# Performance work log

Hardware: AMD Instinct MI355X
Metric: run time of the kernel (lower is better)

Reference implementation:

```python
import jax, jax.numpy as jnp
import numpy as np

B, C, HC, H, W = 4, 512, 64, 64, 64


def _spectral_norm(Wm, u):
    # one torch-style power iteration; u,v are treated as constants (detached)
    v = Wm.T @ u
    v = v / jnp.maximum(jnp.linalg.norm(v), 1e-12)
    u2 = Wm @ v
    u2 = u2 / jnp.maximum(jnp.linalg.norm(u2), 1e-12)
    u2 = jax.lax.stop_gradient(u2)
    v = jax.lax.stop_gradient(v)
    sigma = u2 @ (Wm @ v)
    return Wm / sigma


def setup_inputs() -> dict:
    key = jax.random.key(0)
    ks = jax.random.split(key, 14)
    return {
        "x": jax.random.normal(ks[0], (B, C, H, W), jnp.float32),
        "Wf": jax.random.normal(ks[1], (HC, C), jnp.float32) * 0.05,
        "bf": jax.random.normal(ks[2], (HC,), jnp.float32) * 0.05,
        "Wg": jax.random.normal(ks[3], (HC, C), jnp.float32) * 0.05,
        "bg": jax.random.normal(ks[4], (HC,), jnp.float32) * 0.05,
        "Wh": jax.random.normal(ks[5], (HC, C), jnp.float32) * 0.05,
        "bh": jax.random.normal(ks[6], (HC,), jnp.float32) * 0.05,
        "Wv": jax.random.normal(ks[7], (C, HC), jnp.float32) * 0.05,
        "bv": jax.random.normal(ks[8], (C,), jnp.float32) * 0.05,
        "uf": jax.random.normal(ks[9], (HC,), jnp.float32),
        "ug": jax.random.normal(ks[10], (HC,), jnp.float32),
        "uh": jax.random.normal(ks[11], (HC,), jnp.float32),
        "uv": jax.random.normal(ks[12], (C,), jnp.float32),
        "gamma": jax.random.normal(ks[13], (1,), jnp.float32),
    }


def reference(x, Wf, bf, Wg, bg, Wh, bh, Wv, bv, uf, ug, uh, uv, gamma):
    nb, nc, imgh, imgw = x.shape
    n = imgh * imgw
    xf = x.reshape(nb, nc, n)  # [B, C, N]
    Wf_sn = _spectral_norm(Wf, uf)
    Wg_sn = _spectral_norm(Wg, ug)
    Wh_sn = _spectral_norm(Wh, uh)
    Wv_sn = _spectral_norm(Wv, uv)
    # 1x1 convs are per-pixel GEMMs
    f = jnp.einsum('kc,bcn->bkn', Wf_sn, xf) + bf[:, None]  # [B, HC, N]
    g = jnp.einsum('kc,bcn->bkn', Wg_sn, xf) + bg[:, None]
    h = jnp.einsum('kc,bcn->bkn', Wh_sn, xf) + bh[:, None]
    s = jnp.einsum('bkn,bkm->bnm', f, g)       # [B, N, N] scores
    beta = jax.nn.softmax(s, axis=-1)
    o = jnp.einsum('bnm,bkm->bkn', beta, h)    # [B, HC, N] (already transposed)
    out = jnp.einsum('ck,bkn->bcn', Wv_sn, o) + bv[:, None]
    out = out.reshape(nb, nc, imgh, imgw)
    return gamma[0] * out + x
```

## Files before the change

kernel.cpp:

```cpp
#include <hip/hip_runtime.h>
#include <hip/hip_bf16.h>

typedef __attribute__((ext_vector_type(8))) short short8;
typedef __attribute__((ext_vector_type(4))) float floatx4;
typedef __attribute__((ext_vector_type(16))) float floatx16;
typedef unsigned short ushortt;

#define LOG2E 1.4426950408889634f

__device__ __forceinline__ float fast_exp2(float x) {
    return __builtin_amdgcn_exp2f(x);
}
__device__ __forceinline__ ushortt f2bf(float f) {
    unsigned int u = __float_as_uint(f);
    u += 0x7fffu + ((u >> 16) & 1u);
    return (ushortt)(u >> 16);
}
__device__ __forceinline__ unsigned int f2bf_pk(float a, float b) {
    float2 t; t.x = a; t.y = b;
    __hip_bfloat162 h = __float22bfloat162_rn(t);
    return *reinterpret_cast<unsigned int*>(&h);
}
__device__ __forceinline__ float bf2f(ushortt h) {
    return __uint_as_float(((unsigned int)h) << 16);
}

__device__ __forceinline__ float block_sum(float v, float* red) {
    #pragma unroll
    for (int off = 32; off > 0; off >>= 1) v += __shfl_down(v, off);
    int wid = threadIdx.x >> 6, ln = threadIdx.x & 63;
    __syncthreads();
    if (ln == 0) red[wid] = v;
    __syncthreads();
    return red[0] + red[1] + red[2] + red[3];
}

__global__ __launch_bounds__(256) void sigma_kernel(
    const float* __restrict__ Wf, const float* __restrict__ uf,
    const float* __restrict__ Wg, const float* __restrict__ ug,
    const float* __restrict__ Wh, const float* __restrict__ uh,
    const float* __restrict__ Wv, const float* __restrict__ uv,
    float* __restrict__ sig) {
    __shared__ float tv[512];
    __shared__ float tvp[256];
    __shared__ float zpart[256];
    __shared__ float red[4];
    const int mat = blockIdx.x, tid = threadIdx.x;

    if (mat < 3) {
        const float* W = (mat == 0) ? Wf : ((mat == 1) ? Wg : Wh);
        const float* u = (mat == 0) ? uf : ((mat == 1) ? ug : uh);
        for (int c = tid; c < 512; c += 256) {
            float s0 = 0.f;
            #pragma unroll 8
            for (int r = 0; r < 64; ++r) s0 += W[r * 512 + c] * u[r];
            tv[c] = s0;
        }
        __syncthreads();
        float p = tv[tid] * tv[tid] + tv[tid + 256] * tv[tid + 256];
        float nt2 = block_sum(p, red);
        float nt = fmaxf(sqrtf(nt2), 1e-12f);
        {
            int r = tid & 63, qq = tid >> 6;
            const float* Wr = W + r * 512 + qq * 128;
            const float* tq = tv + qq * 128;
            float part = 0.f;
            #pragma unroll 16
            for (int c = 0; c < 128; ++c) part += Wr[c] * tq[c];
            zpart[tid] = part;
        }
        __syncthreads();
        if (tid < 64) {
            float z = zpart[tid] + zpart[tid + 64] + zpart[tid + 128] + zpart[tid + 192];
            z = z * z;
            #pragma unroll
            for (int off = 32; off > 0; off >>= 1) z += __shfl_xor(z, off);
            if (tid == 0) sig[mat] = sqrtf(z) / nt;
        }
    } else {
        const float* W = Wv; const float* u = uv;
        {
            int c = tid & 63, rs = tid >> 6;
            float s0 = 0.f;
            #pragma unroll 8
            for (int r = rs * 128; r < rs * 128 + 128; ++r) s0 += W[r * 64 + c] * u[r];
            tvp[tid] = s0;
        }
        __syncthreads();
        if (tid < 64) tv[tid] = tvp[tid] + tvp[tid + 64] + tvp[tid + 128] + tvp[tid + 192];
        __syncthreads();
        float t = (tid < 64) ? tv[tid] : 0.f;
        float nt2 = block_sum(t * t, red);
        float nt = fmaxf(sqrtf(nt2), 1e-12f);
        {
            const float* w1 = W + (size_t)tid * 64;
            const float* w2 = W + (size_t)(tid + 256) * 64;
            float z1 = 0.f, z2 = 0.f;
            #pragma unroll 8
            for (int c = 0; c < 64; ++c) {
                float tc = tv[c];
                z1 += w1[c] * tc;
                z2 += w2[c] * tc;
            }
            float zp = z1 * z1 + z2 * z2;
            float z2t = block_sum(zp, red);
            if (tid == 0) sig[3] = sqrtf(z2t) / nt;
        }
    }
}

__global__ __launch_bounds__(256) void prep_w_kernel(
    const float* __restrict__ Wf, const float* __restrict__ Wg,
    const float* __restrict__ Wh, const float* __restrict__ Wv,
    const float* __restrict__ sig,
    ushortt* __restrict__ wqkv, ushortt* __restrict__ wvb) {
    int idx = blockIdx.x * 256 + threadIdx.x;
    if (idx < 98304) {
        int k = idx >> 9, c = idx & 511;
        int which = k >> 6;
        const float* W = (which == 0) ? Wf : ((which == 1) ? Wg : Wh);
        float inv = 1.0f / sig[which];
        wqkv[idx] = f2bf(W[(k & 63) * 512 + c] * inv);
    } else {
        int o = idx - 98304;
        wvb[o] = f2bf(Wv[o] / sig[3]);
    }
}

__global__ __launch_bounds__(256, 4) void qkv_kernel(
    const float* __restrict__ x, const ushortt* __restrict__ wqkv,
    const float* __restrict__ bfv, const float* __restrict__ bgv,
    const float* __restrict__ bhv,
    ushortt* __restrict__ Qb, ushortt* __restrict__ Kb, ushortt* __restrict__ Vt) {
    __shared__ unsigned int xs[2048];
    const int tid = threadIdx.x;
    const int n0 = blockIdx.x * 32, b = blockIdx.y;
    const int lane = tid & 63, w = tid >> 6;
    const int strip = w & 1, ksel = w >> 1;
    const int q = lane >> 4, l15 = lane & 15;
    const int sn = tid & 31, sg = tid >> 5;

    floatx4 acc[6];
    #pragma unroll
    for (int kt = 0; kt < 6; ++kt) acc[kt] = (floatx4){0.f, 0.f, 0.f, 0.f};

    const float* xb = x + ((size_t)b * 512) * 4096 + n0 + sn;
    const int sslot = sn * 32 + ((sg ^ (sn & 7)) << 2);
    float2 pre[4];
    #pragma unroll
    for (int i = 0; i < 4; ++i) {
        int c = sg * 8 + 2 * i;
        pre[i].x = xb[(size_t)c * 4096];
        pre[i].y = xb[(size_t)(c + 1) * 4096];
    }
    {
        uint4 pk;
        pk.x = f2bf_pk(pre[0].x, pre[0].y);
        pk.y = f2bf_pk(pre[1].x, pre[1].y);
        pk.z = f2bf_pk(pre[2].x, pre[2].y);
        pk.w = f2bf_pk(pre[3].x, pre[3].y);
        *reinterpret_cast<uint4*>(&xs[sslot]) = pk;
    }
    #pragma unroll
    for (int i = 0; i < 4; ++i) {
        int c = 64 + sg * 8 + 2 * i;
        pre[i].x = xb[(size_t)c * 4096];
        pre[i].y = xb[(size_t)(c + 1) * 4096];
    }

    for (int it = 0; it < 8; ++it) {
        __syncthreads();
        if (it < 7) {
            uint4 pk;
            pk.x = f2bf_pk(pre[0].x, pre[0].y);
            pk.y = f2bf_pk(pre[1].x, pre[1].y);
            pk.z = f2bf_pk(pre[2].x, pre[2].y);
            pk.w = f2bf_pk(pre[3].x, pre[3].y);
            *reinterpret_cast<uint4*>(&xs[(((it + 1) & 1) << 10) + sslot]) = pk;
        }
        if (it < 6) {
            #pragma unroll
            for (int i = 0; i < 4; ++i) {
                int c = (it + 2) * 64 + sg * 8 + 2 * i;
                pre[i].x = xb[(size_t)c * 4096];
                pre[i].y = xb[(size_t)(c + 1) * 4096];
            }
        }
        const int c0 = it * 64;
        const unsigned int* xr = &xs[((it & 1) << 10) + (16 * strip + l15) * 32];
        #pragma unroll
        for (int kc = 0; kc < 2; ++kc) {
            union { uint4 v; short8 s8; } af;
            af.v = *reinterpret_cast<const uint4*>(&xr[((4 * kc + q) ^ (l15 & 7)) << 2]);
            #pragma unroll
            for (int kt = 0; kt < 6; ++kt) {
                short8 bb = *reinterpret_cast<const short8*>(
                    &wqkv[(size_t)(ksel * 96 + kt * 16 + l15) * 512 + c0 + kc * 32 + q * 8]);
                acc[kt] = __builtin_amdgcn_mfma_f32_16x16x32_bf16(af.s8, bb, acc[kt], 0, 0, 0);
            }
        }
    }

    const int nloc = n0 + 16 * strip + 4 * q;
    if (ksel == 0) {
        #pragma unroll
        for (int kt = 0; kt < 4; ++kt) {
            int k = kt * 16 + l15;
            float bb = bfv[k];
            #pragma unroll
            for (int r = 0; r < 4; ++r)
                Qb[((size_t)b * 4096 + nloc + r) * 64 + k] = f2bf((acc[kt][r] + bb) * LOG2E);
        }
        #pragma unroll
        for (int kt = 4; kt < 6; ++kt) {
            int k = (kt - 4) * 16 + l15;
            float bb = bgv[k];
            #pragma unroll
            for (int r = 0; r < 4; ++r)
                Kb[((size_t)b * 4096 + nloc + r) * 64 + k] = f2bf(acc[kt][r] + bb);
        }
    } else {
        #pragma unroll
        for (int kt = 0; kt < 2; ++kt) {
            int k = 32 + kt * 16 + l15;
            float bb = bgv[k];
            #pragma unroll
            for (int r = 0; r < 4; ++r)
                Kb[((size_t)b * 4096 + nloc + r) * 64 + k] = f2bf(acc[kt][r] + bb);
        }
    }
    __syncthreads();
    if (ksel == 1) {
        #pragma unroll
        for (int kt = 2; kt < 6; ++kt) {
            int d = (kt - 2) * 16 + l15;
            float bb = bhv[d];
            int base = d * 17 + 8 * strip + 2 * q;
            xs[base]     = f2bf_pk(acc[kt][0] + bb, acc[kt][1] + bb);
            xs[base + 1] = f2bf_pk(acc[kt][2] + bb, acc[kt][3] + bb);
        }
    }
    __syncthreads();
    {
        int d = tid >> 2, sgg = tid & 3;
        uint4 vv;
        vv.x = xs[d * 17 + sgg * 4 + 0]; vv.y = xs[d * 17 + sgg * 4 + 1];
        vv.z = xs[d * 17 + sgg * 4 + 2]; vv.w = xs[d * 17 + sgg * 4 + 3];
        *reinterpret_cast<uint4*>(&Vt[((size_t)b * 64 + d) * 4096 + n0 + sgg * 8]) = vv;
    }
}

__global__ __launch_bounds__(256, 3) void attn_kernel(
    const ushortt* __restrict__ Qb, const ushortt* __restrict__ Kb,
    const ushortt* __restrict__ Vt, ushortt* __restrict__ Opart,
    float2* __restrict__ ml, ushortt* __restrict__ Ob, int KB) {
    __shared__ unsigned int smem[8448];
    const int tid = threadIdx.x;
    const int n0 = blockIdx.x * 64, b = blockIdx.y, s = blockIdx.z;
    const int lane = tid & 63, w = tid >> 6;
    const int qh = w & 1, kh = w >> 1;
    const int l31 = lane & 31, h = lane >> 5;

    const ushortt* Kg = Kb + (size_t)b * 4096 * 64;
    const ushortt* Vg = Vt + (size_t)b * 64 * 4096;

    short8 bq[4];
    {
        const ushortt* Qg = Qb + ((size_t)b * 4096 + n0 + 32 * qh + l31) * 64;
        #pragma unroll
        for (int kc = 0; kc < 4; ++kc)
            bq[kc] = *reinterpret_cast<const short8*>(Qg + kc * 16 + 8 * h);
    }

    floatx16 ot0 = {}, ot1 = {};
    float m_i = -1e30f, l_i = 0.f;

    const int row = tid >> 2, seg = tid & 3;
    const int kbeg = s * KB, kend = kbeg + KB;
    const int rsw = row & 7;
    const int ws0 = row * 32 + ((((2 * seg)) ^ rsw) << 2);
    const int ws1 = row * 32 + ((((2 * seg + 1)) ^ rsw) << 2);

    uint4 ck0, ck1, cv0, cv1;
    {
        int nb = kbeg * 64;
        const ushortt* kp = Kg + (size_t)(nb + row) * 64 + seg * 16;
        ck0 = *reinterpret_cast<const uint4*>(kp);
        ck1 = *reinterpret_cast<const uint4*>(kp + 8);
        const ushortt* vp = Vg + (size_t)row * 4096 + nb + seg * 16;
        cv0 = *reinterpret_cast<const uint4*>(vp);
        cv1 = *reinterpret_cast<const uint4*>(vp + 8);
    }
    *reinterpret_cast<uint4*>(&smem[ws0]) = ck0;
    *reinterpret_cast<uint4*>(&smem[ws1]) = ck1;
    *reinterpret_cast<uint4*>(&smem[2048 + ws0]) = cv0;
    *reinterpret_cast<uint4*>(&smem[2048 + ws1]) = cv1;
    if (kbeg + 1 < kend) {
        int nb = (kbeg + 1) * 64;
        const ushortt* kp = Kg + (size_t)(nb + row) * 64 + seg * 16;
        ck0 = *reinterpret_cast<const uint4*>(kp);
        ck1 = *reinterpret_cast<const uint4*>(kp + 8);
        const ushortt* vp = Vg + (size_t)row * 4096 + nb + seg * 16;
        cv0 = *reinterpret_cast<const uint4*>(vp);
        cv1 = *reinterpret_cast<const uint4*>(vp + 8);
    }

    for (int kb = kbeg; kb < kend; ++kb) {
        const int cur = (kb - kbeg) & 1;
        const unsigned int rb = cur ? 4096u : 0u;
        const unsigned int wbs = cur ? 0u : 4096u;
        __syncthreads();
        if (kb + 1 < kend) {
            *reinterpret_cast<uint4*>(&smem[wbs + ws0]) = ck0;
            *reinterpret_cast<uint4*>(&smem[wbs + ws1]) = ck1;
            *reinterpret_cast<uint4*>(&smem[wbs + 2048 + ws0]) = cv0;
            *reinterpret_cast<uint4*>(&smem[wbs + 2048 + ws1]) = cv1;
        }
        if (kb + 2 < kend) {
            int nb = (kb + 2) * 64;
            const ushortt* kp = Kg + (size_t)(nb + row) * 64 + seg * 16;
            ck0 = *reinterpret_cast<const uint4*>(kp);
            ck1 = *reinterpret_cast<const uint4*>(kp + 8);
            const ushortt* vp = Vg + (size_t)row * 4096 + nb + seg * 16;
            cv0 = *reinterpret_cast<const uint4*>(vp);
            cv1 = *reinterpret_cast<const uint4*>(vp + 8);
        }

        floatx16 st = {};
        const unsigned int* kr = &smem[rb + (32 * kh + l31) * 32];
        const int esw = l31 & 7;
        #pragma unroll
        for (int kc = 0; kc < 4; ++kc) {
            union { uint4 v; short8 s8; } af;
            af.v = *reinterpret_cast<const uint4*>(&kr[((2 * kc + h) ^ esw) << 2]);
            st = __builtin_amdgcn_mfma_f32_32x32x16_bf16(af.s8, bq[kc], st, 0, 0, 0);
        }

        float mx = fmaxf(fmaxf(fmaxf(st[0], st[1]), fmaxf(st[2], st[3])),
                         fmaxf(fmaxf(st[4], st[5]), fmaxf(st[6], st[7])));
        float mx2 = fmaxf(fmaxf(fmaxf(st[8], st[9]), fmaxf(st[10], st[11])),
                          fmaxf(fmaxf(st[12], st[13]), fmaxf(st[14], st[15])));
        mx = fmaxf(mx, mx2);
        mx = fmaxf(mx, __shfl_xor(mx, 32));
        if (!__all(mx <= m_i + 8.f)) {
            float mn = fmaxf(m_i, mx);
            float alpha = fast_exp2(m_i - mn);
            m_i = mn;
            l_i *= alpha;
            #pragma unroll
            for (int r = 0; r < 16; ++r) { ot0[r] *= alpha; ot1[r] *= alpha; }
        }
        float p[16], rs = 0.f;
        #pragma unroll
        for (int r = 0; r < 16; ++r) { p[r] = fast_exp2(st[r] - m_i); rs += p[r]; }
        rs += __shfl_xor(rs, 32);
        l_i += rs;

        unsigned int pk[8], sp[8];
        #pragma unroll
        for (int i = 0; i < 8; ++i) pk[i] = f2bf_pk(p[2 * i], p[2 * i + 1]);
        #pragma unroll
        for (int i = 0; i < 8; ++i) sp[i] = (unsigned int)__shfl_xor((int)pk[i], 32);
        union { unsigned int u[4]; short8 s8; } pb0, pb1;
        pb0.u[0] = h ? sp[2] : pk[0]; pb0.u[1] = h ? sp[3] : pk[1];
        pb0.u[2] = h ? pk[2] : sp[0]; pb0.u[3] = h ? pk[3] : sp[1];
        pb1.u[0] = h ? sp[6] : pk[4]; pb1.u[1] = h ? sp[7] : pk[5];
        pb1.u[2] = h ? pk[6] : sp[4]; pb1.u[3] = h ? pk[7] : sp[5];

        const unsigned int* vr0 = &smem[rb + 2048 + l31 * 32];
        const unsigned int* vr1 = &smem[rb + 2048 + (32 + l31) * 32];
        #pragma unroll
        for (int c = 0; c < 2; ++c) {
            union { uint4 v; short8 s8; } af;
            af.v = *reinterpret_cast<const uint4*>(&vr0[((4 * kh + 2 * c + h) ^ esw) << 2]);
            ot0 = __builtin_amdgcn_mfma_f32_32x32x16_bf16(af.s8, c ? pb1.s8 : pb0.s8, ot0, 0, 0, 0);
            af.v = *reinterpret_cast<const uint4*>(&vr1[((4 * kh + 2 * c + h) ^ esw) << 2]);
            ot1 = __builtin_amdgcn_mfma_f32_32x32x16_bf16(af.s8, c ? pb1.s8 : pb0.s8, ot1, 0, 0, 0);
        }
    }

    __syncthreads();
    if (h == 0) {
        smem[8192 + w * 32 + l31] = __float_as_uint(m_i);
        smem[8320 + w * 32 + l31] = __float_as_uint(l_i);
    }
    __syncthreads();
    int pw = 2 * (1 - kh) + qh;
    float m2 = __uint_as_float(smem[8192 + pw * 32 + l31]);
    float l2 = __uint_as_float(smem[8320 + pw * 32 + l31]);
    float mstar = fmaxf(m_i, m2);
    float wself = fast_exp2(m_i - mstar);
    float w2 = fast_exp2(m2 - mstar);
    float lm = wself * l_i + w2 * l2;
    float sc = (gridDim.z == 1) ? (wself / lm) : wself;
    if (gridDim.z > 1 && kh == 0 && h == 0) {
        float2 v; v.x = mstar; v.y = lm;
        ml[((size_t)s * 4 + b) * 4096 + n0 + 32 * qh + l31] = v;
    }
    float* om = reinterpret_cast<float*>(smem);
    if (kh == 0) {
        #pragma unroll
        for (int r = 0; r < 16; ++r) {
            int d0 = (r & 3) + 8 * (r >> 2) + 4 * h;
            om[(32 * qh + l31) * 65 + d0] = sc * ot0[r];
            om[(32 * qh + l31) * 65 + 32 + d0] = sc * ot1[r];
        }
    }
    __syncthreads();
    if (kh == 1) {
        #pragma unroll
        for (int r = 0; r < 16; ++r) {
            int d0 = (r & 3) + 8 * (r >> 2) + 4 * h;
            om[(32 * qh + l31) * 65 + d0] += sc * ot0[r];
            om[(32 * qh + l31) * 65 + 32 + d0] += sc * ot1[r];
        }
    }
    __syncthreads();
    {
        int qq = tid >> 2, dsg = tid & 3;
        unsigned int pkk[8];
        #pragma unroll
        for (int j = 0; j < 8; ++j)
            pkk[j] = f2bf_pk(om[qq * 65 + dsg * 16 + 2 * j], om[qq * 65 + dsg * 16 + 2 * j + 1]);
        ushortt* base = (gridDim.z == 1)
            ? (Ob + ((size_t)b * 4096 + n0) * 64)
            : (Opart + (((size_t)s * 4 + b) * 4096 + n0) * 64);
        uint4* d4 = reinterpret_cast<uint4*>(base + (size_t)qq * 64 + dsg * 16);
        uint4 o0; o0.x = pkk[0]; o0.y = pkk[1]; o0.z = pkk[2]; o0.w = pkk[3];
        uint4 o1; o1.x = pkk[4]; o1.y = pkk[5]; o1.z = pkk[6]; o1.w = pkk[7];
        d4[0] = o0; d4[1] = o1;
    }
}

__global__ __launch_bounds__(256) void combine_kernel(
    const ushortt* __restrict__ Opart, const float2* __restrict__ ml,
    ushortt* __restrict__ Ob, int S) {
    const int tid = threadIdx.x;
    const int n0 = blockIdx.x * 64, b = blockIdx.y;
    const int row = n0 + (tid >> 2), dseg = tid & 3;
    float2 mls[4];
    float m = -1e30f;
    for (int s = 0; s < S; ++s) {
        mls[s] = ml[((size_t)s * 4 + b) * 4096 + row];
        m = fmaxf(m, mls[s].x);
    }
    float wgt[4], denom = 0.f;
    for (int s = 0; s < S; ++s) {
        wgt[s] = fast_exp2(mls[s].x - m);
        denom += wgt[s] * mls[s].y;
    }
    float inv = 1.0f / denom;
    float acc[16];
    #pragma unroll
    for (int j = 0; j < 16; ++j) acc[j] = 0.f;
    for (int s = 0; s < S; ++s) {
        const uint4* op = reinterpret_cast<const uint4*>(
            Opart + (((size_t)s * 4 + b) * 4096 + row) * 64 + dseg * 16);
        union { uint4 v; ushortt hh[8]; } u0, u1;
        u0.v = op[0]; u1.v = op[1];
        float ww = wgt[s];
        #pragma unroll
        for (int j = 0; j < 8; ++j) {
            acc[j] += ww * bf2f(u0.hh[j]);
            acc[8 + j] += ww * bf2f(u1.hh[j]);
        }
    }
    union { uint4 u[2]; unsigned int ww[8]; } pkv;
    #pragma unroll
    for (int j = 0; j < 8; ++j) pkv.ww[j] = f2bf_pk(acc[2 * j] * inv, acc[2 * j + 1] * inv);
    uint4* dst = reinterpret_cast<uint4*>(Ob + ((size_t)b * 4096 + row) * 64 + dseg * 16);
    dst[0] = pkv.u[0]; dst[1] = pkv.u[1];
}

__global__ __launch_bounds__(256) void proj_kernel(
    const ushortt* __restrict__ Ob, const ushortt* __restrict__ wvb,
    const float* __restrict__ bv, const float* __restrict__ gamma,
    const float* __restrict__ x, float* __restrict__ out) {
    __shared__ float ps[64 * 65];
    const int tid = threadIdx.x;
    const int n0 = blockIdx.y * 64, c0 = blockIdx.x * 64, b = blockIdx.z;
    const int w = tid >> 6, lane = tid & 63, q = lane >> 4, l15 = lane & 15;

    short8 a0 = *reinterpret_cast<const short8*>(&wvb[(size_t)(c0 + 16 * w + l15) * 64 + q * 8]);
    short8 a1 = *reinterpret_cast<const short8*>(&wvb[(size_t)(c0 + 16 * w + l15) * 64 + 32 + q * 8]);
    floatx4 acc[4];
    #pragma unroll
    for (int t = 0; t < 4; ++t) acc[t] = (floatx4){0.f, 0.f, 0.f, 0.f};
    #pragma unroll
    for (int t = 0; t < 4; ++t) {
        const ushortt* ob = Ob + ((size_t)b * 4096 + n0 + 16 * t + l15) * 64;
        short8 b0 = *reinterpret_cast<const short8*>(ob + q * 8);
        short8 b1 = *reinterpret_cast<const short8*>(ob + 32 + q * 8);
        acc[t] = __builtin_amdgcn_mfma_f32_16x16x32_bf16(a0, b0, acc[t], 0, 0, 0);
        acc[t] = __builtin_amdgcn_mfma_f32_16x16x32_bf16(a1, b1, acc[t], 0, 0, 0);
    }
    #pragma unroll
    for (int t = 0; t < 4; ++t) {
        #pragma unroll
        for (int r = 0; r < 4; ++r)
            ps[(16 * w + 4 * q + r) * 65 + 16 * t + l15] = acc[t][r];
    }
    __syncthreads();
    float gm = gamma[0];
    const int cl = tid >> 4;
    const int n4 = (tid & 15) * 4;
    #pragma unroll
    for (int p = 0; p < 4; ++p) {
        int c = c0 + p * 16 + cl;
        float bb = bv[c];
        size_t idx = ((size_t)(b * 512 + c)) * 4096 + n0 + n4;
        float4 xv = *reinterpret_cast<const float4*>(&x[idx]);
        const float* pr = &ps[(p * 16 + cl) * 65 + n4];
        float4 ov;
        ov.x = gm * (pr[0] + bb) + xv.x;
        ov.y = gm * (pr[1] + bb) + xv.y;
        ov.z = gm * (pr[2] + bb) + xv.z;
        ov.w = gm * (pr[3] + bb) + xv.w;
        *reinterpret_cast<float4*>(&out[idx]) = ov;
    }
}

extern "C" void kernel_launch(void* const* d_in, const int* in_sizes, int n_in,
                              void* d_out, int out_size, void* d_ws, size_t ws_size,
                              hipStream_t stream) {
    const float* x   = (const float*)d_in[0];
    const float* Wf  = (const float*)d_in[1];
    const float* bf_ = (const float*)d_in[2];
    const float* Wg  = (const float*)d_in[3];
    const float* bg_ = (const float*)d_in[4];
    const float* Wh  = (const float*)d_in[5];
    const float* bh_ = (const float*)d_in[6];
    const float* Wv  = (const float*)d_in[7];
    const float* bv_ = (const float*)d_in[8];
    const float* uf  = (const float*)d_in[9];
    const float* ug  = (const float*)d_in[10];
    const float* uh  = (const float*)d_in[11];
    const float* uv  = (const float*)d_in[12];
    const float* gm  = (const float*)d_in[13];
    float* out = (float*)d_out;

    char* ws = (char*)d_ws;
    float*   sig   = (float*)ws;
    ushortt* wqkv  = (ushortt*)(ws + 256);
    ushortt* wvb   = (ushortt*)(ws + 196864);
    ushortt* Qb    = (ushortt*)(ws + 262400);
    ushortt* Kb    = (ushortt*)(ws + 2359552);
    ushortt* Vt    = (ushortt*)(ws + 4456704);
    ushortt* Ob    = (ushortt*)(ws + 6553856);
    float2*  ml    = (float2*)(ws + 8651008);
    ushortt* Opart = (ushortt*)(ws + 9175296);

    int S = (ws_size >= (size_t)17563904) ? 4 : 1;

    sigma_kernel<<<4, 256, 0, stream>>>(Wf, uf, Wg, ug, Wh, uh, Wv, uv, sig);
    prep_w_kernel<<<512, 256, 0, stream>>>(Wf, Wg, Wh, Wv, sig, wqkv, wvb);
    qkv_kernel<<<dim3(128, 4), 256, 0, stream>>>(x, wqkv, bf_, bg_, bh_, Qb, Kb, Vt);
    attn_kernel<<<dim3(64, 4, S), 256, 0, stream>>>(Qb, Kb, Vt, Opart, ml, Ob, 64 / S);
    if (S > 1) combine_kernel<<<dim3(64, 4), 256, 0, stream>>>(Opart, ml, Ob, S);
    proj_kernel<<<dim3(8, 64, 4), 256, 0, stream>>>(Ob, wvb, bv_, gm, x, out);
}
```

Measured before the change: 216.6 us.

## Fuse weight prep into sigma kernel and split-combine into projection kernel

After: 189.4 us. 1.14x faster.

```diff
diff --git a/kernel.cpp b/kernel.cpp
--- a/kernel.cpp
+++ b/kernel.cpp
@@ -40,11 +40,13 @@
     const float* __restrict__ Wg, const float* __restrict__ ug,
     const float* __restrict__ Wh, const float* __restrict__ uh,
     const float* __restrict__ Wv, const float* __restrict__ uv,
-    float* __restrict__ sig) {
+    float* __restrict__ sig,
+    ushortt* __restrict__ wqkv, ushortt* __restrict__ wvb) {
     __shared__ float tv[512];
     __shared__ float tvp[256];
     __shared__ float zpart[256];
     __shared__ float red[4];
+    __shared__ float ssig;
     const int mat = blockIdx.x, tid = threadIdx.x;
 
     if (mat < 3) {
@@ -75,7 +77,20 @@
             z = z * z;
             #pragma unroll
             for (int off = 32; off > 0; off >>= 1) z += __shfl_xor(z, off);
-            if (tid == 0) sig[mat] = sqrtf(z) / nt;
+            if (tid == 0) {
+                float sg0 = sqrtf(z) / nt;
+                sig[mat] = sg0;
+                ssig = sg0;
+            }
+        }
+        __syncthreads();
+        float inv = 1.0f / ssig;
+        const float4* W4 = reinterpret_cast<const float4*>(W);
+        unsigned int* dst = reinterpret_cast<unsigned int*>(wqkv + mat * 32768);
+        for (int i = tid; i < 8192; i += 256) {
+            float4 wv = W4[i];
+            dst[2 * i]     = f2bf_pk(wv.x * inv, wv.y * inv);
+            dst[2 * i + 1] = f2bf_pk(wv.z * inv, wv.w * inv);
         }
     } else {
         const float* W = Wv; const float* u = uv;
@@ -92,6 +107,7 @@
         float t = (tid < 64) ? tv[tid] : 0.f;
         float nt2 = block_sum(t * t, red);
         float nt = fmaxf(sqrtf(nt2), 1e-12f);
+        float sg3;
         {
             const float* w1 = W + (size_t)tid * 64;
             const float* w2 = W + (size_t)(tid + 256) * 64;
@@ -104,26 +120,17 @@
             }
             float zp = z1 * z1 + z2 * z2;
             float z2t = block_sum(zp, red);
-            if (tid == 0) sig[3] = sqrtf(z2t) / nt;
-        }
-    }
-}
-
-__global__ __launch_bounds__(256) void prep_w_kernel(
-    const float* __restrict__ Wf, const float* __restrict__ Wg,
-    const float* __restrict__ Wh, const float* __restrict__ Wv,
-    const float* __restrict__ sig,
-    ushortt* __restrict__ wqkv, ushortt* __restrict__ wvb) {
-    int idx = blockIdx.x * 256 + threadIdx.x;
-    if (idx < 98304) {
-        int k = idx >> 9, c = idx & 511;
-        int which = k >> 6;
-        const float* W = (which == 0) ? Wf : ((which == 1) ? Wg : Wh);
-        float inv = 1.0f / sig[which];
-        wqkv[idx] = f2bf(W[(k & 63) * 512 + c] * inv);
-    } else {
-        int o = idx - 98304;
-        wvb[o] = f2bf(Wv[o] / sig[3]);
+            sg3 = sqrtf(z2t) / nt;
+            if (tid == 0) sig[3] = sg3;
+        }
+        float inv = 1.0f / sg3;
+        const float4* W4 = reinterpret_cast<const float4*>(W);
+        unsigned int* dst = reinterpret_cast<unsigned int*>(wvb);
+        for (int i = tid; i < 8192; i += 256) {
+            float4 wv = W4[i];
+            dst[2 * i]     = f2bf_pk(wv.x * inv, wv.y * inv);
+            dst[2 * i + 1] = f2bf_pk(wv.z * inv, wv.w * inv);
+        }
     }
 }
 
@@ -432,91 +439,102 @@
     }
 }
 
-__global__ __launch_bounds__(256) void combine_kernel(
+__global__ __launch_bounds__(256, 2) void proj_kernel(
     const ushortt* __restrict__ Opart, const float2* __restrict__ ml,
-    ushortt* __restrict__ Ob, int S) {
-    const int tid = threadIdx.x;
-    const int n0 = blockIdx.x * 64, b = blockIdx.y;
-    const int row = n0 + (tid >> 2), dseg = tid & 3;
-    float2 mls[4];
-    float m = -1e30f;
-    for (int s = 0; s < S; ++s) {
-        mls[s] = ml[((size_t)s * 4 + b) * 4096 + row];
-        m = fmaxf(m, mls[s].x);
-    }
-    float wgt[4], denom = 0.f;
-    for (int s = 0; s < S; ++s) {
-        wgt[s] = fast_exp2(mls[s].x - m);
-        denom += wgt[s] * mls[s].y;
-    }
-    float inv = 1.0f / denom;
-    float acc[16];
-    #pragma unroll
-    for (int j = 0; j < 16; ++j) acc[j] = 0.f;
-    for (int s = 0; s < S; ++s) {
-        const uint4* op = reinterpret_cast<const uint4*>(
-            Opart + (((size_t)s * 4 + b) * 4096 + row) * 64 + dseg * 16);
-        union { uint4 v; ushortt hh[8]; } u0, u1;
-        u0.v = op[0]; u1.v = op[1];
-        float ww = wgt[s];
-        #pragma unroll
-        for (int j = 0; j < 8; ++j) {
-            acc[j] += ww * bf2f(u0.hh[j]);
-            acc[8 + j] += ww * bf2f(u1.hh[j]);
-        }
-    }
-    union { uint4 u[2]; unsigned int ww[8]; } pkv;
-    #pragma unroll
-    for (int j = 0; j < 8; ++j) pkv.ww[j] = f2bf_pk(acc[2 * j] * inv, acc[2 * j + 1] * inv);
-    uint4* dst = reinterpret_cast<uint4*>(Ob + ((size_t)b * 4096 + row) * 64 + dseg * 16);
-    dst[0] = pkv.u[0]; dst[1] = pkv.u[1];
-}
-
-__global__ __launch_bounds__(256) void proj_kernel(
     const ushortt* __restrict__ Ob, const ushortt* __restrict__ wvb,
     const float* __restrict__ bv, const float* __restrict__ gamma,
-    const float* __restrict__ x, float* __restrict__ out) {
-    __shared__ float ps[64 * 65];
+    const float* __restrict__ x, float* __restrict__ out, int S) {
+    __shared__ ushortt ol[32 * 72];
     const int tid = threadIdx.x;
-    const int n0 = blockIdx.y * 64, c0 = blockIdx.x * 64, b = blockIdx.z;
+    const int n0 = blockIdx.x * 32, b = blockIdx.y;
+
+    {
+        int row = tid >> 3, t8 = tid & 7;
+        int rg = n0 + row;
+        if (S == 1) {
+            uint4 v = *reinterpret_cast<const uint4*>(
+                Ob + ((size_t)b * 4096 + rg) * 64 + t8 * 8);
+            *reinterpret_cast<uint4*>(&ol[row * 72 + t8 * 8]) = v;
+        } else {
+            float2 mls[4];
+            float m = -1e30f;
+            #pragma unroll 4
+            for (int s = 0; s < 4; ++s) {
+                mls[s] = ml[((size_t)s * 4 + b) * 4096 + rg];
+                m = fmaxf(m, mls[s].x);
+            }
+            float wgt[4], denom = 0.f;
+            #pragma unroll 4
+            for (int s = 0; s < 4; ++s) {
+                wgt[s] = fast_exp2(mls[s].x - m);
+                denom += wgt[s] * mls[s].y;
+            }
+            float inv = 1.0f / denom;
+            float acc[8];
+            #pragma unroll
+            for (int j = 0; j < 8; ++j) acc[j] = 0.f;
+            #pragma unroll 4
+            for (int s = 0; s < 4; ++s) {
+                union { uint4 v; ushortt hh[8]; } u;
+                u.v = *reinterpret_cast<const uint4*>(
+                    Opart + (((size_t)s * 4 + b) * 4096 + rg) * 64 + t8 * 8);
+                float ww = wgt[s];
+                #pragma unroll
+                for (int j = 0; j < 8; ++j) acc[j] += ww * bf2f(u.hh[j]);
+            }
+            uint4 v;
+            v.x = f2bf_pk(acc[0] * inv, acc[1] * inv);
+            v.y = f2bf_pk(acc[2] * inv, acc[3] * inv);
+            v.z = f2bf_pk(acc[4] * inv, acc[5] * inv);
+            v.w = f2bf_pk(acc[6] * inv, acc[7] * inv);
+            *reinterpret_cast<uint4*>(&ol[row * 72 + t8 * 8]) = v;
+        }
+    }
+    __syncthreads();
+
     const int w = tid >> 6, lane = tid & 63, q = lane >> 4, l15 = lane & 15;
-
-    short8 a0 = *reinterpret_cast<const short8*>(&wvb[(size_t)(c0 + 16 * w + l15) * 64 + q * 8]);
-    short8 a1 = *reinterpret_cast<const short8*>(&wvb[(size_t)(c0 + 16 * w + l15) * 64 + 32 + q * 8]);
-    floatx4 acc[4];
-    #pragma unroll
-    for (int t = 0; t < 4; ++t) acc[t] = (floatx4){0.f, 0.f, 0.f, 0.f};
-    #pragma unroll
-    for (int t = 0; t < 4; ++t) {
-        const ushortt* ob = Ob + ((size_t)b * 4096 + n0 + 16 * t + l15) * 64;
-        short8 b0 = *reinterpret_cast<const short8*>(ob + q * 8);
-        short8 b1 = *reinterpret_cast<const short8*>(ob + 32 + q * 8);
-        acc[t] = __builtin_amdgcn_mfma_f32_16x16x32_bf16(a0, b0, acc[t], 0, 0, 0);
-        acc[t] = __builtin_amdgcn_mfma_f32_16x16x32_bf16(a1, b1, acc[t], 0, 0, 0);
-    }
-    #pragma unroll
-    for (int t = 0; t < 4; ++t) {
-        #pragma unroll
-        for (int r = 0; r < 4; ++r)
-            ps[(16 * w + 4 * q + r) * 65 + 16 * t + l15] = acc[t][r];
-    }
-    __syncthreads();
+    short8 bfr[2][2];
+    #pragma unroll
+    for (int u = 0; u < 2; ++u)
+        #pragma unroll
+        for (int kc = 0; kc < 2; ++kc)
+            bfr[u][kc] = *reinterpret_cast<const short8*>(
+                &ol[(16 * u + l15) * 72 + 32 * kc + q * 8]);
+
+    floatx4 acc[8][2];
+    #pragma unroll
+    for (int t = 0; t < 8; ++t)
+        #pragma unroll
+        for (int u = 0; u < 2; ++u) acc[t][u] = (floatx4){0.f, 0.f, 0.f, 0.f};
+
+    const int cw = w * 128;
+    #pragma unroll
+    for (int t = 0; t < 8; ++t) {
+        short8 a0 = *reinterpret_cast<const short8*>(
+            &wvb[(size_t)(cw + 16 * t + l15) * 64 + q * 8]);
+        short8 a1 = *reinterpret_cast<const short8*>(
+            &wvb[(size_t)(cw + 16 * t + l15) * 64 + 32 + q * 8]);
+        #pragma unroll
+        for (int u = 0; u < 2; ++u) {
+            acc[t][u] = __builtin_amdgcn_mfma_f32_16x16x32_bf16(a0, bfr[u][0], acc[t][u], 0, 0, 0);
+            acc[t][u] = __builtin_amdgcn_mfma_f32_16x16x32_bf16(a1, bfr[u][1], acc[t][u], 0, 0, 0);
+        }
+    }
+
     float gm = gamma[0];
-    const int cl = tid >> 4;
-    const int n4 = (tid & 15) * 4;
-    #pragma unroll
-    for (int p = 0; p < 4; ++p) {
-        int c = c0 + p * 16 + cl;
-        float bb = bv[c];
-        size_t idx = ((size_t)(b * 512 + c)) * 4096 + n0 + n4;
-        float4 xv = *reinterpret_cast<const float4*>(&x[idx]);
-        const float* pr = &ps[(p * 16 + cl) * 65 + n4];
-        float4 ov;
-        ov.x = gm * (pr[0] + bb) + xv.x;
-        ov.y = gm * (pr[1] + bb) + xv.y;
-        ov.z = gm * (pr[2] + bb) + xv.z;
-        ov.w = gm * (pr[3] + bb) + xv.w;
-        *reinterpret_cast<float4*>(&out[idx]) = ov;
+    #pragma unroll
+    for (int t = 0; t < 8; ++t) {
+        #pragma unroll
+        for (int r = 0; r < 4; ++r) {
+            int c = cw + 16 * t + 4 * q + r;
+            float bb = bv[c];
+            #pragma unroll
+            for (int u = 0; u < 2; ++u) {
+                int n = n0 + 16 * u + l15;
+                size_t idx = ((size_t)(b * 512 + c)) * 4096 + n;
+                out[idx] = gm * (acc[t][u][r] + bb) + x[idx];
+            }
+        }
     }
 }
 
@@ -552,10 +570,8 @@
 
     int S = (ws_size >= (size_t)17563904) ? 4 : 1;
 
-    sigma_kernel<<<4, 256, 0, stream>>>(Wf, uf, Wg, ug, Wh, uh, Wv, uv, sig);
-    prep_w_kernel<<<512, 256, 0, stream>>>(Wf, Wg, Wh, Wv, sig, wqkv, wvb);
+    sigma_kernel<<<4, 256, 0, stream>>>(Wf, uf, Wg, ug, Wh, uh, Wv, uv, sig, wqkv, wvb);
     qkv_kernel<<<dim3(128, 4), 256, 0, stream>>>(x, wqkv, bf_, bg_, bh_, Qb, Kb, Vt);
     attn_kernel<<<dim3(64, 4, S), 256, 0, stream>>>(Qb, Kb, Vt, Opart, ml, Ob, 64 / S);
-    if (S > 1) combine_kernel<<<dim3(64, 4), 256, 0, stream>>>(Opart, ml, Ob, S);
-    proj_kernel<<<dim3(8, 64, 4), 256, 0, stream>>>(Ob, wvb, bv_, gm, x, out);
-}
+    proj_kernel<<<dim3(128, 4), 256, 0, stream>>>(Opart, ml, Ob, wvb, bv_, gm, x, out, S);
+}
```
